# Kernel tuning notes

Hardware: AMD Instinct MI355X
Metric: run time of the kernel (lower is better)

## Reference

```python
import jax, jax.numpy as jnp
import numpy as np

H = 256  # hidden_size
D = 256  # in_vocab_size
T = 512  # sequence length


def setup_inputs() -> dict:
    key = jax.random.key(0)
    k1, k2, k3, k4, k5 = jax.random.split(key, 5)
    # faithful param init from the torch module
    u1 = jax.random.uniform(k1, (H,), minval=1e-4, maxval=1.0)
    u2 = jax.random.uniform(k2, (H,), minval=1e-4, maxval=1.0)
    lamda = jnp.log(-0.5 * jnp.log(u1))
    theta = jnp.log(6.28 * u2)
    B_c1 = jax.random.normal(k3, (H, D), dtype=jnp.float32) / np.float32(np.sqrt(D))
    B_c2 = jax.random.normal(k4, (H, D), dtype=jnp.float32) / np.float32(np.sqrt(D))
    x_sequence = jax.random.normal(k5, (T, D), dtype=jnp.float32)
    return {"x_sequence": x_sequence, "lamda": lamda, "theta": theta,
            "B_c1": B_c1, "B_c2": B_c2}


def reference(x_sequence, lamda, theta, B_c1, B_c2):
    Hh = lamda.shape[0]
    Dd = B_c1.shape[1]
    # per-step constant coefficients (depend only on params)
    y = jnp.exp(-jnp.exp(lamda))
    z = jnp.exp(theta)
    gamma = jnp.sqrt(1.0 - y * y)
    cz, sz = jnp.cos(z), jnp.sin(z)
    c, s = y * cz, y * sz                       # rotation coefficients [H]
    y_g = -jnp.exp(lamda) * y                   # dy/dlamda
    gamma_g = -y / gamma * y_g                  # dgamma/dlamda
    z_g = jnp.exp(theta)                        # dz/dtheta
    # precompute input projections for all steps: [T, H]
    Bx1 = x_sequence @ B_c1.T
    Bx2 = x_sequence @ B_c2.T

    def step(carry, xs):
        h1, h2, sr1, sr2, st1, st2, sB11, sB12, sB21, sB22 = carry
        x_t, bx1, bx2 = xs
        # hidden state (complex diagonal rotation, split into 2 real channels)
        h1n = c * h1 - s * h2 + gamma * bx1
        h2n = c * h2 + s * h1 + gamma * bx2
        # RTRL sensitivities w.r.t. lamda
        sr1n = y_g * cz * h1 + c * sr1 - y_g * sz * h2 - s * sr2 + gamma_g * bx1
        sr2n = y_g * cz * h2 + c * sr2 + y_g * sz * h1 + s * sr1 + gamma_g * bx2
        # RTRL sensitivities w.r.t. theta
        st1n = -s * z_g * h1 + c * st1 - c * z_g * h2 - s * st2
        st2n = -s * z_g * h2 + c * st2 + c * z_g * h1 + s * st1
        # RTRL sensitivities w.r.t. B matrices, [H, D]
        gx = gamma[:, None] * x_t[None, :]
        sB11n = c[:, None] * sB11 - s[:, None] * sB12 + gx
        sB12n = c[:, None] * sB12 + s[:, None] * sB11
        sB21n = c[:, None] * sB21 - s[:, None] * sB22
        sB22n = c[:, None] * sB22 + s[:, None] * sB21 + gx
        out = jnp.concatenate([h1n, h2n])       # [2H]
        return (h1n, h2n, sr1n, sr2n, st1n, st2n, sB11n, sB12n, sB21n, sB22n), out

    zv = jnp.zeros((Hh,), jnp.float32)
    zm = jnp.zeros((Hh, Dd), jnp.float32)
    init = (zv, zv, zv, zv, zv, zv, zm, zm, zm, zm)
    _, outs = jax.lax.scan(step, init, (x_sequence, Bx1, Bx2))
    return outs  # [T, 2H]
```

## Files before the change

kernel.cpp:

```cpp
#include <hip/hip_runtime.h>

#define TT 512
#define DD 256
#define HH 256
#define CC 128
#define LL (TT / CC)

__device__ inline void coeffs(const float* __restrict__ lamda,
                              const float* __restrict__ theta, int j,
                              float& c, float& s, float& g) {
  const float y = __expf(-__expf(lamda[j]));
  const float z = __expf(theta[j]);
  c = y * __cosf(z);
  s = y * __sinf(z);
  g = sqrtf(fmaxf(1.0f - y * y, 0.0f));
}

__global__ __launch_bounds__(256) void rtu_chunk(
    const float* __restrict__ x, const float* __restrict__ lamda,
    const float* __restrict__ theta, const float* __restrict__ B1,
    const float* __restrict__ B2, float* __restrict__ out,
    float* __restrict__ E) {
  __shared__ float xs[LL][DD];
  const int cidx = blockIdx.x;
  const int t0 = cidx * LL;
  const int j = threadIdx.x;

  {
    const float4* xsrc = (const float4*)(x + t0 * DD);
    ((float4*)(&xs[0][0]))[j] = xsrc[j];
  }
  __syncthreads();

  const float4* b1 = (const float4*)(B1 + j * DD);
  const float4* b2 = (const float4*)(B2 + j * DD);
  const float4* xs4 = (const float4*)(&xs[0][0]);

  float a1[LL], a2[LL];
#pragma unroll
  for (int tt = 0; tt < LL; ++tt) { a1[tt] = 0.f; a2[tt] = 0.f; }

#pragma unroll 8
  for (int k4 = 0; k4 < DD / 4; ++k4) {
    float4 v1 = b1[k4];
    float4 v2 = b2[k4];
#pragma unroll
    for (int tt = 0; tt < LL; ++tt) {
      float4 xv = xs4[tt * (DD / 4) + k4];
      a1[tt] = fmaf(v1.x, xv.x, a1[tt]);
      a1[tt] = fmaf(v1.y, xv.y, a1[tt]);
      a1[tt] = fmaf(v1.z, xv.z, a1[tt]);
      a1[tt] = fmaf(v1.w, xv.w, a1[tt]);
      a2[tt] = fmaf(v2.x, xv.x, a2[tt]);
      a2[tt] = fmaf(v2.y, xv.y, a2[tt]);
      a2[tt] = fmaf(v2.z, xv.z, a2[tt]);
      a2[tt] = fmaf(v2.w, xv.w, a2[tt]);
    }
  }

  float c, s, g;
  coeffs(lamda, theta, j, c, s, g);

  float h1 = 0.f, h2 = 0.f;
#pragma unroll
  for (int tt = 0; tt < LL; ++tt) {
    const float bb1 = a1[tt] * g;
    const float bb2 = a2[tt] * g;
    const float n1 = fmaf(c, h1, fmaf(-s, h2, bb1));
    const float n2 = fmaf(c, h2, fmaf(s, h1, bb2));
    h1 = n1;
    h2 = n2;
    out[(t0 + tt) * (2 * HH) + j] = h1;
    out[(t0 + tt) * (2 * HH) + HH + j] = h2;
  }
  E[cidx * (2 * HH) + j] = h1;
  E[cidx * (2 * HH) + HH + j] = h2;
}

__global__ __launch_bounds__(256) void rtu_fixup(
    const float* __restrict__ lamda, const float* __restrict__ theta,
    const float* __restrict__ E, float* __restrict__ out) {
  const int cidx = blockIdx.x;
  if (cidx == 0) return;
  const int j = threadIdx.x;
  float c, s, g;
  coeffs(lamda, theta, j, c, s, g);

  float cl = c, sl = s;
#pragma unroll
  for (int q = 0; q < 2; ++q) {
    const float nc = cl * cl - sl * sl;
    const float ns = 2.f * cl * sl;
    cl = nc;
    sl = ns;
  }

  float S1 = 0.f, S2 = 0.f;
  const float* Ep = E + j;
#pragma unroll 8
  for (int ci = 0; ci < cidx; ++ci) {
    const float E1 = Ep[ci * (2 * HH)];
    const float E2 = Ep[ci * (2 * HH) + HH];
    const float n1 = fmaf(cl, S1, fmaf(-sl, S2, E1));
    const float n2 = fmaf(cl, S2, fmaf(sl, S1, E2));
    S1 = n1;
    S2 = n2;
  }

  const int t0 = cidx * LL;
  float p1 = c, p2 = s;
#pragma unroll
  for (int i = 0; i < LL; ++i) {
    const int t = t0 + i;
    const float o1 = out[t * (2 * HH) + j] + p1 * S1 - p2 * S2;
    const float o2 = out[t * (2 * HH) + HH + j] + p2 * S1 + p1 * S2;
    out[t * (2 * HH) + j] = o1;
    out[t * (2 * HH) + HH + j] = o2;
    const float np1 = p1 * c - p2 * s;
    const float np2 = p1 * s + p2 * c;
    p1 = np1;
    p2 = np2;
  }
}

extern "C" void kernel_launch(void* const* d_in, const int* in_sizes, int n_in,
                              void* d_out, int out_size, void* d_ws, size_t ws_size,
                              hipStream_t stream) {
  const float* x     = (const float*)d_in[0];
  const float* lamda = (const float*)d_in[1];
  const float* theta = (const float*)d_in[2];
  const float* B1    = (const float*)d_in[3];
  const float* B2    = (const float*)d_in[4];
  float* out = (float*)d_out;

  float* E = (float*)d_ws;

  rtu_chunk<<<dim3(CC), 256, 0, stream>>>(x, lamda, theta, B1, B2, out, E);
  rtu_fixup<<<dim3(CC), 256, 0, stream>>>(lamda, theta, E, out);
}
```

Measured before the change: 87.32 us.

## Split chunk projection over hidden units and K with shuffle reduction

Chunks drop from 128 to 32, each 16 steps long. The projection is then split across 8 blocks per chunk by hidden-unit groups, and within each block across 8 lanes along the reduction dimension, with a wave-shuffle reduction at the end. A rotated K index staggers shared-memory accesses, and output stores are spread across the K lanes. The aim is more parallel work and less redundant B reading per block, while keeping the two-pass chunked scan. The cost is a longer serial recurrence per chunk and extra shuffle work.

```diff
diff --git a/kernel.cpp b/kernel.cpp
--- a/kernel.cpp
+++ b/kernel.cpp
@@ -3,8 +3,13 @@
 #define TT 512
 #define DD 256
 #define HH 256
-#define CC 128
+
+#define CC 32
 #define LL (TT / CC)
+#define USPLIT 8
+#define UPB (HH / USPLIT)
+#define KSPLIT 8
+#define KW (DD / KSPLIT)
 
 __device__ inline void coeffs(const float* __restrict__ lamda,
                               const float* __restrict__ theta, int j,
@@ -21,32 +26,40 @@
     const float* __restrict__ theta, const float* __restrict__ B1,
     const float* __restrict__ B2, float* __restrict__ out,
     float* __restrict__ E) {
-  __shared__ float xs[LL][DD];
-  const int cidx = blockIdx.x;
+  __shared__ float xs[LL * DD];
+  const int cidx = blockIdx.x >> 3;
+  const int q = blockIdx.x & (USPLIT - 1);
   const int t0 = cidx * LL;
-  const int j = threadIdx.x;
+  const int tid = threadIdx.x;
+  const int ul = tid >> 3;
+  const int kq = tid & (KSPLIT - 1);
+  const int u = q * UPB + ul;
 
   {
     const float4* xsrc = (const float4*)(x + t0 * DD);
-    ((float4*)(&xs[0][0]))[j] = xsrc[j];
+    float4* xdst = (float4*)xs;
+#pragma unroll
+    for (int p = 0; p < (LL * DD / 4) / 256; ++p)
+      xdst[p * 256 + tid] = xsrc[p * 256 + tid];
   }
   __syncthreads();
 
-  const float4* b1 = (const float4*)(B1 + j * DD);
-  const float4* b2 = (const float4*)(B2 + j * DD);
-  const float4* xs4 = (const float4*)(&xs[0][0]);
+  const float4* b1 = (const float4*)(B1 + u * DD + kq * KW);
+  const float4* b2 = (const float4*)(B2 + u * DD + kq * KW);
+  const float4* xs4 = (const float4*)xs;
 
   float a1[LL], a2[LL];
 #pragma unroll
   for (int tt = 0; tt < LL; ++tt) { a1[tt] = 0.f; a2[tt] = 0.f; }
 
-#pragma unroll 8
-  for (int k4 = 0; k4 < DD / 4; ++k4) {
-    float4 v1 = b1[k4];
-    float4 v2 = b2[k4];
+#pragma unroll
+  for (int k4 = 0; k4 < KW / 4; ++k4) {
+    const int kk = (k4 + kq) & (KW / 4 - 1);
+    const float4 v1 = b1[kk];
+    const float4 v2 = b2[kk];
 #pragma unroll
     for (int tt = 0; tt < LL; ++tt) {
-      float4 xv = xs4[tt * (DD / 4) + k4];
+      const float4 xv = xs4[tt * (DD / 4) + kq * (KW / 4) + kk];
       a1[tt] = fmaf(v1.x, xv.x, a1[tt]);
       a1[tt] = fmaf(v1.y, xv.y, a1[tt]);
       a1[tt] = fmaf(v1.z, xv.z, a1[tt]);
@@ -58,8 +71,21 @@
     }
   }
 
+#pragma unroll
+  for (int tt = 0; tt < LL; ++tt) {
+    float r1 = a1[tt], r2 = a2[tt];
+    r1 += __shfl_xor(r1, 1);
+    r1 += __shfl_xor(r1, 2);
+    r1 += __shfl_xor(r1, 4);
+    r2 += __shfl_xor(r2, 1);
+    r2 += __shfl_xor(r2, 2);
+    r2 += __shfl_xor(r2, 4);
+    a1[tt] = r1;
+    a2[tt] = r2;
+  }
+
   float c, s, g;
-  coeffs(lamda, theta, j, c, s, g);
+  coeffs(lamda, theta, u, c, s, g);
 
   float h1 = 0.f, h2 = 0.f;
 #pragma unroll
@@ -70,11 +96,13 @@
     const float n2 = fmaf(c, h2, fmaf(s, h1, bb2));
     h1 = n1;
     h2 = n2;
-    out[(t0 + tt) * (2 * HH) + j] = h1;
-    out[(t0 + tt) * (2 * HH) + HH + j] = h2;
+    if (kq == (tt >> 1)) {
+      out[(t0 + tt) * (2 * HH) + u] = h1;
+      out[(t0 + tt) * (2 * HH) + HH + u] = h2;
+    }
   }
-  E[cidx * (2 * HH) + j] = h1;
-  E[cidx * (2 * HH) + HH + j] = h2;
+  if (kq == 0) E[cidx * (2 * HH) + u] = h1;
+  if (kq == 1) E[cidx * (2 * HH) + HH + u] = h2;
 }
 
 __global__ __launch_bounds__(256) void rtu_fixup(
@@ -88,7 +116,7 @@
 
   float cl = c, sl = s;
 #pragma unroll
-  for (int q = 0; q < 2; ++q) {
+  for (int qq = 0; qq < 4; ++qq) {
     const float nc = cl * cl - sl * sl;
     const float ns = 2.f * cl * sl;
     cl = nc;
@@ -135,6 +163,7 @@
 
   float* E = (float*)d_ws;
 
-  rtu_chunk<<<dim3(CC), 256, 0, stream>>>(x, lamda, theta, B1, B2, out, E);
+  rtu_chunk<<<dim3(CC * USPLIT), 256, 0, stream>>>(x, lamda, theta, B1, B2,
+                                                   out, E);
   rtu_fixup<<<dim3(CC), 256, 0, stream>>>(lamda, theta, E, out);
 }
```

New measurement: 78.13 us. -10.5%, faster.
